# Optimization experiments

Hardware: AMD Instinct MI355X
Metric: run time of the kernel (lower is better)

The kernel has to match this reference:

```python
import jax, jax.numpy as jnp
import numpy as np

N_NODES = 100000
IN_FEATURES = 128
OUT_FEATURES = 128
N_EDGES = 3200000


def setup_inputs() -> dict:
    key = jax.random.key(0)
    k1, k2, k3, k4, k5 = jax.random.split(key, 5)
    node_features = jax.random.normal(k1, (N_NODES, IN_FEATURES), dtype=jnp.float32)
    edge_index = jax.random.randint(k2, (2, N_EDGES), 0, N_NODES, dtype=jnp.int64)
    edge_values = jax.random.uniform(k3, (N_EDGES,), dtype=jnp.float32)
    # Linear layer params (PyTorch nn.Linear: y = x @ W.T + b)
    bound = 1.0 / np.sqrt(IN_FEATURES)
    W = jax.random.uniform(k4, (OUT_FEATURES, IN_FEATURES), minval=-bound, maxval=bound, dtype=jnp.float32)
    b = jax.random.uniform(k5, (OUT_FEATURES,), minval=-bound, maxval=bound, dtype=jnp.float32)
    return {"node_features": node_features, "edge_index": edge_index,
            "edge_values": edge_values, "W": W, "b": b}


def reference(node_features, edge_index, edge_values, W, b):
    n_nodes = node_features.shape[0]
    row, col = edge_index[0], edge_index[1]
    # zero diagonal entries, then square edge values
    vals = jnp.where(row != col, edge_values, jnp.zeros_like(edge_values)) ** 2
    # linear transform: [N, F_out]
    wx = node_features @ W.T + b
    # SpMM: temp[i] = sum_e vals[e] * wx[col[e]] for row[e] == i
    messages = vals[:, None] * wx[col]          # [E, F_out] gather + scale
    temp = jax.ops.segment_sum(messages, row, num_segments=n_nodes)  # scatter-add
    # Hadamard product
    return wx * temp
```

## Files before the change

### kernel.cpp

```cpp
#include <hip/hip_runtime.h>
#include <hip/hip_bf16.h>

#define F 128
#define RB 196
#define NB_MAX 511
#define BIN_CAP 16
#define NBLK_BIN 512
#define NXS 16
#define NCG 16
#define KEYS (RB * NCG)

typedef __attribute__((ext_vector_type(8))) short bf16x8;
typedef __attribute__((ext_vector_type(4))) float f32x4;

static __device__ __forceinline__ unsigned short f2bfbits(float f) {
    __hip_bfloat16 h = __float2bfloat16(f);
    return __builtin_bit_cast(unsigned short, h);
}
static __device__ __forceinline__ short f2bf(float f) {
    __hip_bfloat16 h = __float2bfloat16(f);
    return __builtin_bit_cast(short, h);
}

__global__ __launch_bounds__(256) void gemm_mfma_kernel(
    const float* __restrict__ X, const float* __restrict__ W,
    const float* __restrict__ bias, float* __restrict__ wxf,
    __hip_bfloat16* __restrict__ wxh, int nrows, int writeF)
{
    __shared__ short xs[128][136];
    __shared__ short wt[128][136];
    __shared__ float bsh[128];

    int t = threadIdx.x;
    long row0 = (long)blockIdx.x * 128;

    {
        int r = t >> 1, h = t & 1;
        const float4* src = reinterpret_cast<const float4*>(W + r * F + h * 64);
#pragma unroll
        for (int i = 0; i < 16; ++i) {
            float4 v = src[i];
            short4 s;
            s.x = f2bf(v.x); s.y = f2bf(v.y); s.z = f2bf(v.z); s.w = f2bf(v.w);
            *reinterpret_cast<short4*>(&wt[r][h * 64 + i * 4]) = s;
        }
        if (t < 128) bsh[t] = bias[t];
    }
    {
        int r = t >> 1, h = t & 1;
        long gr = row0 + r; if (gr > nrows - 1) gr = nrows - 1;
        const float4* src = reinterpret_cast<const float4*>(X + gr * F + h * 64);
#pragma unroll
        for (int i = 0; i < 16; ++i) {
            float4 v = src[i];
            short4 s;
            s.x = f2bf(v.x); s.y = f2bf(v.y); s.z = f2bf(v.z); s.w = f2bf(v.w);
            *reinterpret_cast<short4*>(&xs[r][h * 64 + i * 4]) = s;
        }
    }
    __syncthreads();

    int wave = t >> 6, lane = t & 63;
    int l15 = lane & 15, lg = lane >> 4;
    int mrow = wave * 32;

    float bj[8];
#pragma unroll
    for (int nf = 0; nf < 8; ++nf) bj[nf] = bsh[nf * 16 + l15];

    f32x4 acc[2][8] = {};

#pragma unroll
    for (int ks = 0; ks < 4; ++ks) {
        bf16x8 a0 = *reinterpret_cast<const bf16x8*>(&xs[mrow + l15][ks * 32 + lg * 8]);
        bf16x8 a1 = *reinterpret_cast<const bf16x8*>(&xs[mrow + 16 + l15][ks * 32 + lg * 8]);
#pragma unroll
        for (int nf = 0; nf < 8; ++nf) {
            bf16x8 bfr = *reinterpret_cast<const bf16x8*>(&wt[nf * 16 + l15][ks * 32 + lg * 8]);
            acc[0][nf] = __builtin_amdgcn_mfma_f32_16x16x32_bf16(a0, bfr, acc[0][nf], 0, 0, 0);
            acc[1][nf] = __builtin_amdgcn_mfma_f32_16x16x32_bf16(a1, bfr, acc[1][nf], 0, 0, 0);
        }
    }

#pragma unroll
    for (int mf = 0; mf < 2; ++mf) {
#pragma unroll
        for (int i = 0; i < 4; ++i) {
            long grow = row0 + mrow + mf * 16 + lg * 4 + i;
            if (grow < nrows) {
#pragma unroll
                for (int nf = 0; nf < 8; ++nf) {
                    float v = acc[mf][nf][i] + bj[nf];
                    int col = nf * 16 + l15;
                    wxh[grow * F + col] = __float2bfloat16(v);
                    if (writeF) wxf[grow * F + col] = v;
                }
            }
        }
    }
}

__global__ __launch_bounds__(256) void bin_edges_kernel(
    const int* __restrict__ rowi, const int* __restrict__ coli,
    const float* __restrict__ ev, int* __restrict__ cur2,
    int2* __restrict__ arena1, int E, int NB, int CAPX)
{
    __shared__ int2 bins[NB_MAX][BIN_CAP];
    __shared__ int  cnt[NB_MAX];
    __shared__ int  flushed[NB_MAX];

    int t = threadIdx.x;
    int x = blockIdx.x & (NXS - 1);
    for (int i = t; i < NB; i += 256) { cnt[i] = 0; flushed[i] = 0; }
    __syncthreads();

    long per   = ((long)E + NBLK_BIN - 1) / NBLK_BIN;
    long start = (long)blockIdx.x * per;
    long endE  = start + per; if (endE > E) endE = E;

    int r = 0, c = 0; float v = 0.f;
    {
        long i0 = start + t;
        if (i0 < endE) { r = rowi[i0]; c = coli[i0]; v = ev[i0]; }
    }

    for (long base = start; base < endE; base += 256) {
        if (base + t < endE) {
            float v2 = (r != c) ? v * v : 0.0f;
            int b  = r / RB;
            int rl = r - b * RB;
            int pos = atomicAdd(&cnt[b], 1);
            bins[b][pos & (BIN_CAP - 1)] = make_int2((rl << 17) | c, __float_as_int(v2));
        }
        int rn = 0, cn = 0; float vn = 0.f;
        {
            long i2 = base + 256 + t;
            if (i2 < endE) { rn = rowi[i2]; cn = coli[i2]; vn = ev[i2]; }
        }
        __syncthreads();
        for (int bb = t; bb < NB; bb += 256) {
            while (cnt[bb] - flushed[bb] >= 8) {
                int gpos = atomicAdd(&cur2[x * NB + bb], 8);
                if (gpos + 8 <= CAPX) {
                    const int2* src = &bins[bb][flushed[bb] & (BIN_CAP - 1)];
                    int2* dst = &arena1[((size_t)x * NB + bb) * CAPX + gpos];
                    const int4* s4 = (const int4*)src;
                    int4* d4 = (int4*)dst;
                    d4[0] = s4[0]; d4[1] = s4[1]; d4[2] = s4[2]; d4[3] = s4[3];
                }
                flushed[bb] += 8;
            }
        }
        __syncthreads();
        r = rn; c = cn; v = vn;
    }
    for (int bb = t; bb < NB; bb += 256) {
        int rem = cnt[bb] - flushed[bb];
        if (rem > 0) {
            int gpos = atomicAdd(&cur2[x * NB + bb], rem);
            if (gpos + rem <= CAPX) {
                int2* dst = &arena1[((size_t)x * NB + bb) * CAPX + gpos];
                for (int k = 0; k < rem; ++k)
                    dst[k] = bins[bb][(flushed[bb] + k) & (BIN_CAP - 1)];
            }
        }
    }
}

__global__ __launch_bounds__(256) void sort_bucket_kernel(
    const int* __restrict__ cur2, const int2* __restrict__ arena1,
    unsigned int* __restrict__ arena2, int2* __restrict__ rowoff,
    int nrows, int NB, int CAPX, int CAP)
{
    __shared__ int koff[KEYS];
    __shared__ int sscan[256];

    int b = blockIdx.x;
    int t = threadIdx.x;
    unsigned int* dst = arena2 + (size_t)b * CAP;

    for (int i = t; i < KEYS; i += 256) koff[i] = 0;
    __syncthreads();

    for (int x = 0; x < NXS; ++x) {
        int n_x = cur2[x * NB + b]; if (n_x > CAPX) n_x = CAPX;
        const int2* seg = arena1 + ((size_t)x * NB + b) * CAPX;
        for (int i = t; i < n_x; i += 256) {
            int rx = seg[i].x;
            int key = (rx >> 17) * NCG + ((rx & 0x1FFFF) >> 13);
            atomicAdd(&koff[key], 1);
        }
    }
    __syncthreads();

    const int PER = (KEYS + 255) / 256;
    int lo = t * PER, hi = lo + PER; if (hi > KEYS) hi = KEYS; if (lo > KEYS) lo = KEYS;
    int s = 0;
    for (int i = lo; i < hi; ++i) s += koff[i];
    sscan[t] = s;
    __syncthreads();
#pragma unroll
    for (int d = 1; d < 256; d <<= 1) {
        int u = (t >= d) ? sscan[t - d] : 0;
        __syncthreads();
        sscan[t] += u;
        __syncthreads();
    }
    int total = sscan[255];
    int run = (t == 0) ? 0 : sscan[t - 1];
    for (int i = lo; i < hi; ++i) {
        int c0 = koff[i];
        koff[i] = run;
        run += c0;
    }
    __syncthreads();

    if (t < RB) {
        int grow = b * RB + t;
        if (grow < nrows) {
            int start = koff[t * NCG];
            int end   = (t == RB - 1) ? total : koff[(t + 1) * NCG];
            rowoff[grow] = make_int2(b * CAP + start, b * CAP + end);
        }
    }
    __syncthreads();

    for (int x = 0; x < NXS; ++x) {
        int n_x = cur2[x * NB + b]; if (n_x > CAPX) n_x = CAPX;
        const int2* seg = arena1 + ((size_t)x * NB + b) * CAPX;
        for (int i = t; i < n_x; i += 256) {
            int2 rec = seg[i];
            int c = rec.x & 0x1FFFF;
            int key = (rec.x >> 17) * NCG + (c >> 13);
            int pos = atomicAdd(&koff[key], 1);
            unsigned int pk = ((unsigned int)f2bfbits(__int_as_float(rec.y)) << 17)
                              | (unsigned int)c;
            if (pos < CAP) dst[pos] = pk;
        }
    }
}

__global__ __launch_bounds__(256) void agg_row_kernel(
    const int2* __restrict__ rowoff, const unsigned int* __restrict__ arena2,
    const unsigned int* __restrict__ wxh32, float* __restrict__ out,
    int nrows)
{
    int wid  = (blockIdx.x * 256 + threadIdx.x) >> 6;
    int lane = threadIdx.x & 63;
    if (wid >= nrows) return;

    int2 se   = rowoff[wid];
    int start = __builtin_amdgcn_readfirstlane(se.x);
    int end   = __builtin_amdgcn_readfirstlane(se.y);

    unsigned int gw = wxh32[(size_t)wid * 64 + lane];
    const unsigned int* wl = wxh32 + lane;

    float accx = 0.f, accy = 0.f;
    int e = start;
    for (; e + 7 < end; e += 8) {
        unsigned int p0 = arena2[e];
        unsigned int p1 = arena2[e + 1];
        unsigned int p2 = arena2[e + 2];
        unsigned int p3 = arena2[e + 3];
        unsigned int p4 = arena2[e + 4];
        unsigned int p5 = arena2[e + 5];
        unsigned int p6 = arena2[e + 6];
        unsigned int p7 = arena2[e + 7];
        unsigned int g0 = wl[(size_t)(p0 & 0x1FFFF) * 64];
        unsigned int g1 = wl[(size_t)(p1 & 0x1FFFF) * 64];
        unsigned int g2 = wl[(size_t)(p2 & 0x1FFFF) * 64];
        unsigned int g3 = wl[(size_t)(p3 & 0x1FFFF) * 64];
        unsigned int g4 = wl[(size_t)(p4 & 0x1FFFF) * 64];
        unsigned int g5 = wl[(size_t)(p5 & 0x1FFFF) * 64];
        unsigned int g6 = wl[(size_t)(p6 & 0x1FFFF) * 64];
        unsigned int g7 = wl[(size_t)(p7 & 0x1FFFF) * 64];
        float v0 = __uint_as_float((p0 >> 17) << 16);
        float v1 = __uint_as_float((p1 >> 17) << 16);
        float v2 = __uint_as_float((p2 >> 17) << 16);
        float v3 = __uint_as_float((p3 >> 17) << 16);
        float v4 = __uint_as_float((p4 >> 17) << 16);
        float v5 = __uint_as_float((p5 >> 17) << 16);
        float v6 = __uint_as_float((p6 >> 17) << 16);
        float v7 = __uint_as_float((p7 >> 17) << 16);
        accx = fmaf(v0, __uint_as_float(g0 << 16), accx);
        accy = fmaf(v0, __uint_as_float(g0 & 0xFFFF0000u), accy);
        accx = fmaf(v1, __uint_as_float(g1 << 16), accx);
        accy = fmaf(v1, __uint_as_float(g1 & 0xFFFF0000u), accy);
        accx = fmaf(v2, __uint_as_float(g2 << 16), accx);
        accy = fmaf(v2, __uint_as_float(g2 & 0xFFFF0000u), accy);
        accx = fmaf(v3, __uint_as_float(g3 << 16), accx);
        accy = fmaf(v3, __uint_as_float(g3 & 0xFFFF0000u), accy);
        accx = fmaf(v4, __uint_as_float(g4 << 16), accx);
        accy = fmaf(v4, __uint_as_float(g4 & 0xFFFF0000u), accy);
        accx = fmaf(v5, __uint_as_float(g5 << 16), accx);
        accy = fmaf(v5, __uint_as_float(g5 & 0xFFFF0000u), accy);
        accx = fmaf(v6, __uint_as_float(g6 << 16), accx);
        accy = fmaf(v6, __uint_as_float(g6 & 0xFFFF0000u), accy);
        accx = fmaf(v7, __uint_as_float(g7 << 16), accx);
        accy = fmaf(v7, __uint_as_float(g7 & 0xFFFF0000u), accy);
    }
    for (; e < end; ++e) {
        unsigned int p0 = arena2[e];
        unsigned int g0 = wl[(size_t)(p0 & 0x1FFFF) * 64];
        float v0 = __uint_as_float((p0 >> 17) << 16);
        accx = fmaf(v0, __uint_as_float(g0 << 16), accx);
        accy = fmaf(v0, __uint_as_float(g0 & 0xFFFF0000u), accy);
    }

    float2 o;
    o.x = __uint_as_float(gw << 16) * accx;
    o.y = __uint_as_float(gw & 0xFFFF0000u) * accy;
    *reinterpret_cast<float2*>(out + (size_t)wid * F + lane * 2) = o;
}

__global__ __launch_bounds__(256) void edge_scatter_kernel(
    const int* __restrict__ rowi, const int* __restrict__ coli,
    const float* __restrict__ ev, const float* __restrict__ wx,
    float* __restrict__ temp, int E)
{
    int tid = blockIdx.x * 256 + threadIdx.x;
    int e   = tid >> 5;
    if (e >= E) return;
    int lane = tid & 31;
    int r = rowi[e];
    int c = coli[e];
    if (r == c) return;
    float v = ev[e];
    v = v * v;
    const float4 wv = *reinterpret_cast<const float4*>(wx + (size_t)c * F + lane * 4);
    float* tp = temp + (size_t)r * F + lane * 4;
    atomicAdd(tp + 0, v * wv.x);
    atomicAdd(tp + 1, v * wv.y);
    atomicAdd(tp + 2, v * wv.z);
    atomicAdd(tp + 3, v * wv.w);
}

__global__ __launch_bounds__(256) void finalize_kernel(
    float* __restrict__ out, const float* __restrict__ temp, int n4)
{
    int i = blockIdx.x * 256 + threadIdx.x;
    if (i >= n4) return;
    float4 o  = reinterpret_cast<float4*>(out)[i];
    float4 tv = reinterpret_cast<const float4*>(temp)[i];
    o.x *= tv.x; o.y *= tv.y; o.z *= tv.z; o.w *= tv.w;
    reinterpret_cast<float4*>(out)[i] = o;
}

__global__ void Interaction_GraphConvolution_55963423867450_kernel() {}

extern "C" void kernel_launch(void* const* d_in, const int* in_sizes, int n_in,
                              void* d_out, int out_size, void* d_ws, size_t ws_size,
                              hipStream_t stream)
{
    const float* X  = (const float*)d_in[0];
    const int*   ei = (const int*)d_in[1];
    const float* ev = (const float*)d_in[2];
    const float* W  = (const float*)d_in[3];
    const float* b  = (const float*)d_in[4];
    float* out = (float*)d_out;

    int nrows = in_sizes[0] / F;
    int E     = in_sizes[2];
    const int* rowi = ei;
    const int* coli = ei + E;

    int gblocks = (int)((nrows + 127) / 128);

    int NB = (nrows + RB - 1) / RB;
    if (NB <= NB_MAX && nrows < (1 << 17)) {
        long avg = (long)E / NB;
        int CAP  = (int)(((avg * 9) / 8 + 192 + 7) & ~7L);
        int CAPX = (int)(((avg / NXS) * 5 / 4 + 64 + 7) & ~7L);

        char* p = (char*)d_ws;
        __hip_bfloat16* wxh = (__hip_bfloat16*)p;
        p += (size_t)nrows * F * sizeof(__hip_bfloat16);
        int* cur2 = (int*)p;
        p += (size_t)NXS * NB * sizeof(int);
        p = (char*)(((uintptr_t)p + 63) & ~(uintptr_t)63);
        int2* rowoff = (int2*)p;
        p += (size_t)nrows * sizeof(int2);
        int2* arena1 = (int2*)p;
        p += (size_t)NXS * NB * CAPX * sizeof(int2);
        unsigned int* arena2 = (unsigned int*)p;
        p += (size_t)NB * CAP * sizeof(unsigned int);
        size_t need = (size_t)(p - (char*)d_ws);

        if (ws_size >= need) {
            hipMemsetAsync(cur2, 0, (size_t)NXS * NB * sizeof(int), stream);
            gemm_mfma_kernel<<<gblocks, 256, 0, stream>>>(X, W, b, out, wxh, nrows, 0);
            bin_edges_kernel<<<NBLK_BIN, 256, 0, stream>>>(rowi, coli, ev, cur2,
                                                           arena1, E, NB, CAPX);
            sort_bucket_kernel<<<NB, 256, 0, stream>>>(cur2, arena1, arena2,
                                                       rowoff, nrows, NB, CAPX, CAP);
            int ablocks = (int)(((long)nrows * 64 + 255) / 256);
            agg_row_kernel<<<ablocks, 256, 0, stream>>>(rowoff, arena2,
                                                        (const unsigned int*)wxh,
                                                        out, nrows);
            return;
        }
    }

    float* temp = (float*)d_ws;
    hipMemsetAsync(temp, 0, (size_t)nrows * F * sizeof(float), stream);
    __hip_bfloat16* wxh_dummy = (__hip_bfloat16*)((char*)d_ws + (size_t)nrows * F * sizeof(float));
    gemm_mfma_kernel<<<(int)((nrows + 127) / 128), 256, 0, stream>>>(X, W, b, out, wxh_dummy, nrows, 1);
    long ethreads = (long)E * 32;
    int  eblocks32 = (int)((ethreads + 255) / 256);
    edge_scatter_kernel<<<eblocks32, 256, 0, stream>>>(rowi, coli, ev, out, temp, E);
    int n4 = nrows * F / 4;
    finalize_kernel<<<(n4 + 255) / 256, 256, 0, stream>>>(out, temp, n4);
}
```

Measured before the change: 214.2 us.

## Fuse GEMM and edge binning into one kernel, use nontemporal loads/stores

Merges the bf16 MFMA linear transform and the edge-binning pass into a single launch whose blocks take either role by interleaved groups of eight. GEMM blocks become persistent and loop over row tiles. The goal is to overlap the compute-bound GEMM with the memory-bound binning and save a launch. Separately, the streaming reads of the arenas and the final output stores become nontemporal to reduce cache pollution. The risk is that the larger shared-memory footprint lowers occupancy and the role split leaves load imbalance.

```diff
diff --git a/kernel.cpp b/kernel.cpp
--- a/kernel.cpp
+++ b/kernel.cpp
@@ -12,6 +12,8 @@
 
 typedef __attribute__((ext_vector_type(8))) short bf16x8;
 typedef __attribute__((ext_vector_type(4))) float f32x4;
+typedef __attribute__((ext_vector_type(2))) float f32x2;
+typedef __attribute__((ext_vector_type(2))) int   i32x2;
 
 static __device__ __forceinline__ unsigned short f2bfbits(float f) {
     __hip_bfloat16 h = __float2bfloat16(f);
@@ -22,18 +24,17 @@
     return __builtin_bit_cast(short, h);
 }
 
-__global__ __launch_bounds__(256) void gemm_mfma_kernel(
+__device__ __forceinline__ void gemm_role(
+    char* smem, int gid, int ntiles,
     const float* __restrict__ X, const float* __restrict__ W,
     const float* __restrict__ bias, float* __restrict__ wxf,
     __hip_bfloat16* __restrict__ wxh, int nrows, int writeF)
 {
-    __shared__ short xs[128][136];
-    __shared__ short wt[128][136];
-    __shared__ float bsh[128];
+    short (*xs)[136] = reinterpret_cast<short(*)[136]>(smem);
+    short (*wt)[136] = reinterpret_cast<short(*)[136]>(smem + 34816);
+    float* bsh       = reinterpret_cast<float*>(smem + 69632);
 
     int t = threadIdx.x;
-    long row0 = (long)blockIdx.x * 128;
-
     {
         int r = t >> 1, h = t & 1;
         const float4* src = reinterpret_cast<const float4*>(W + r * F + h * 64);
@@ -46,76 +47,81 @@
         }
         if (t < 128) bsh[t] = bias[t];
     }
-    {
-        int r = t >> 1, h = t & 1;
-        long gr = row0 + r; if (gr > nrows - 1) gr = nrows - 1;
-        const float4* src = reinterpret_cast<const float4*>(X + gr * F + h * 64);
-#pragma unroll
-        for (int i = 0; i < 16; ++i) {
-            float4 v = src[i];
-            short4 s;
-            s.x = f2bf(v.x); s.y = f2bf(v.y); s.z = f2bf(v.z); s.w = f2bf(v.w);
-            *reinterpret_cast<short4*>(&xs[r][h * 64 + i * 4]) = s;
-        }
-    }
-    __syncthreads();
 
     int wave = t >> 6, lane = t & 63;
     int l15 = lane & 15, lg = lane >> 4;
     int mrow = wave * 32;
 
-    float bj[8];
-#pragma unroll
-    for (int nf = 0; nf < 8; ++nf) bj[nf] = bsh[nf * 16 + l15];
-
-    f32x4 acc[2][8] = {};
-
-#pragma unroll
-    for (int ks = 0; ks < 4; ++ks) {
-        bf16x8 a0 = *reinterpret_cast<const bf16x8*>(&xs[mrow + l15][ks * 32 + lg * 8]);
-        bf16x8 a1 = *reinterpret_cast<const bf16x8*>(&xs[mrow + 16 + l15][ks * 32 + lg * 8]);
-#pragma unroll
-        for (int nf = 0; nf < 8; ++nf) {
-            bf16x8 bfr = *reinterpret_cast<const bf16x8*>(&wt[nf * 16 + l15][ks * 32 + lg * 8]);
-            acc[0][nf] = __builtin_amdgcn_mfma_f32_16x16x32_bf16(a0, bfr, acc[0][nf], 0, 0, 0);
-            acc[1][nf] = __builtin_amdgcn_mfma_f32_16x16x32_bf16(a1, bfr, acc[1][nf], 0, 0, 0);
-        }
-    }
-
-#pragma unroll
-    for (int mf = 0; mf < 2; ++mf) {
-#pragma unroll
-        for (int i = 0; i < 4; ++i) {
-            long grow = row0 + mrow + mf * 16 + lg * 4 + i;
-            if (grow < nrows) {
-#pragma unroll
-                for (int nf = 0; nf < 8; ++nf) {
-                    float v = acc[mf][nf][i] + bj[nf];
-                    int col = nf * 16 + l15;
-                    wxh[grow * F + col] = __float2bfloat16(v);
-                    if (writeF) wxf[grow * F + col] = v;
+    for (int tile = gid; tile < ntiles; tile += NBLK_BIN) {
+        long row0 = (long)tile * 128;
+        __syncthreads();
+        {
+            int r = t >> 1, h = t & 1;
+            long gr = row0 + r; if (gr > nrows - 1) gr = nrows - 1;
+            const float4* src = reinterpret_cast<const float4*>(X + gr * F + h * 64);
+#pragma unroll
+            for (int i = 0; i < 16; ++i) {
+                float4 v = src[i];
+                short4 s;
+                s.x = f2bf(v.x); s.y = f2bf(v.y); s.z = f2bf(v.z); s.w = f2bf(v.w);
+                *reinterpret_cast<short4*>(&xs[r][h * 64 + i * 4]) = s;
+            }
+        }
+        __syncthreads();
+
+        float bj[8];
+#pragma unroll
+        for (int nf = 0; nf < 8; ++nf) bj[nf] = bsh[nf * 16 + l15];
+
+        f32x4 acc[2][8] = {};
+#pragma unroll
+        for (int ks = 0; ks < 4; ++ks) {
+            bf16x8 a0 = *reinterpret_cast<const bf16x8*>(&xs[mrow + l15][ks * 32 + lg * 8]);
+            bf16x8 a1 = *reinterpret_cast<const bf16x8*>(&xs[mrow + 16 + l15][ks * 32 + lg * 8]);
+#pragma unroll
+            for (int nf = 0; nf < 8; ++nf) {
+                bf16x8 bfr = *reinterpret_cast<const bf16x8*>(&wt[nf * 16 + l15][ks * 32 + lg * 8]);
+                acc[0][nf] = __builtin_amdgcn_mfma_f32_16x16x32_bf16(a0, bfr, acc[0][nf], 0, 0, 0);
+                acc[1][nf] = __builtin_amdgcn_mfma_f32_16x16x32_bf16(a1, bfr, acc[1][nf], 0, 0, 0);
+            }
+        }
+
+#pragma unroll
+        for (int mf = 0; mf < 2; ++mf) {
+#pragma unroll
+            for (int i = 0; i < 4; ++i) {
+                long grow = row0 + mrow + mf * 16 + lg * 4 + i;
+                if (grow < nrows) {
+#pragma unroll
+                    for (int nf = 0; nf < 8; ++nf) {
+                        float v = acc[mf][nf][i] + bj[nf];
+                        int col = nf * 16 + l15;
+                        wxh[grow * F + col] = __float2bfloat16(v);
+                        if (writeF) wxf[grow * F + col] = v;
+                    }
                 }
             }
         }
     }
 }
 
-__global__ __launch_bounds__(256) void bin_edges_kernel(
+__device__ __forceinline__ void bin_role(
+    char* smem, int id,
     const int* __restrict__ rowi, const int* __restrict__ coli,
     const float* __restrict__ ev, int* __restrict__ cur2,
     int2* __restrict__ arena1, int E, int NB, int CAPX)
 {
-    __shared__ int2 bins[NB_MAX][BIN_CAP];
-    __shared__ int  cnt[NB_MAX];
-    __shared__ int  flushed[NB_MAX];
+    int2 (*bins)[BIN_CAP] = reinterpret_cast<int2(*)[BIN_CAP]>(smem);
+    int* cnt     = reinterpret_cast<int*>(smem + 65408);
+    int* flushed = reinterpret_cast<int*>(smem + 65408 + 2048);
 
     int t = threadIdx.x;
-    int x = blockIdx.x & (NXS - 1);
+    int x = id & (NXS - 1);
     for (int i = t; i < NB; i += 256) { cnt[i] = 0; flushed[i] = 0; }
     __syncthreads();
 
     long per   = ((long)E + NBLK_BIN - 1) / NBLK_BIN;
-    long start = (long)blockIdx.x * per;
+    long start = (long)id * per;
     long endE  = start + per; if (endE > E) endE = E;
 
     int r = 0, c = 0; float v = 0.f;
@@ -167,6 +173,33 @@
     }
 }
 
+__global__ __launch_bounds__(256) void fused_gemm_bin_kernel(
+    const float* __restrict__ X, const float* __restrict__ W,
+    const float* __restrict__ bias, __hip_bfloat16* __restrict__ wxh,
+    int nrows, int ntiles,
+    const int* __restrict__ rowi, const int* __restrict__ coli,
+    const float* __restrict__ ev, int* __restrict__ cur2,
+    int2* __restrict__ arena1, int E, int NB, int CAPX)
+{
+    __shared__ __align__(16) char smem[70656];
+    int b = blockIdx.x;
+    int group = b >> 3, within = b & 7;
+    int id = (group >> 1) * 8 + within;
+    if ((group & 1) == 0)
+        bin_role(smem, id, rowi, coli, ev, cur2, arena1, E, NB, CAPX);
+    else
+        gemm_role(smem, id, ntiles, X, W, bias, nullptr, wxh, nrows, 0);
+}
+
+__global__ __launch_bounds__(256) void gemm_mfma_kernel(
+    const float* __restrict__ X, const float* __restrict__ W,
+    const float* __restrict__ bias, float* __restrict__ wxf,
+    __hip_bfloat16* __restrict__ wxh, int nrows, int ntiles, int writeF)
+{
+    __shared__ __align__(16) char smem[70656];
+    gemm_role(smem, blockIdx.x, ntiles, X, W, bias, wxf, wxh, nrows, writeF);
+}
+
 __global__ __launch_bounds__(256) void sort_bucket_kernel(
     const int* __restrict__ cur2, const int2* __restrict__ arena1,
     unsigned int* __restrict__ arena2, int2* __restrict__ rowoff,
@@ -186,7 +219,8 @@
         int n_x = cur2[x * NB + b]; if (n_x > CAPX) n_x = CAPX;
         const int2* seg = arena1 + ((size_t)x * NB + b) * CAPX;
         for (int i = t; i < n_x; i += 256) {
-            int rx = seg[i].x;
+            i32x2 rv = __builtin_nontemporal_load(reinterpret_cast<const i32x2*>(seg + i));
+            int rx = rv[0];
             int key = (rx >> 17) * NCG + ((rx & 0x1FFFF) >> 13);
             atomicAdd(&koff[key], 1);
         }
@@ -229,11 +263,11 @@
         int n_x = cur2[x * NB + b]; if (n_x > CAPX) n_x = CAPX;
         const int2* seg = arena1 + ((size_t)x * NB + b) * CAPX;
         for (int i = t; i < n_x; i += 256) {
-            int2 rec = seg[i];
-            int c = rec.x & 0x1FFFF;
-            int key = (rec.x >> 17) * NCG + (c >> 13);
+            i32x2 rv = __builtin_nontemporal_load(reinterpret_cast<const i32x2*>(seg + i));
+            int c = rv[0] & 0x1FFFF;
+            int key = (rv[0] >> 17) * NCG + (c >> 13);
             int pos = atomicAdd(&koff[key], 1);
-            unsigned int pk = ((unsigned int)f2bfbits(__int_as_float(rec.y)) << 17)
+            unsigned int pk = ((unsigned int)f2bfbits(__int_as_float(rv[1])) << 17)
                               | (unsigned int)c;
             if (pos < CAP) dst[pos] = pk;
         }
@@ -259,14 +293,14 @@
     float accx = 0.f, accy = 0.f;
     int e = start;
     for (; e + 7 < end; e += 8) {
-        unsigned int p0 = arena2[e];
-        unsigned int p1 = arena2[e + 1];
-        unsigned int p2 = arena2[e + 2];
-        unsigned int p3 = arena2[e + 3];
-        unsigned int p4 = arena2[e + 4];
-        unsigned int p5 = arena2[e + 5];
-        unsigned int p6 = arena2[e + 6];
-        unsigned int p7 = arena2[e + 7];
+        unsigned int p0 = __builtin_nontemporal_load(arena2 + e);
+        unsigned int p1 = __builtin_nontemporal_load(arena2 + e + 1);
+        unsigned int p2 = __builtin_nontemporal_load(arena2 + e + 2);
+        unsigned int p3 = __builtin_nontemporal_load(arena2 + e + 3);
+        unsigned int p4 = __builtin_nontemporal_load(arena2 + e + 4);
+        unsigned int p5 = __builtin_nontemporal_load(arena2 + e + 5);
+        unsigned int p6 = __builtin_nontemporal_load(arena2 + e + 6);
+        unsigned int p7 = __builtin_nontemporal_load(arena2 + e + 7);
         unsigned int g0 = wl[(size_t)(p0 & 0x1FFFF) * 64];
         unsigned int g1 = wl[(size_t)(p1 & 0x1FFFF) * 64];
         unsigned int g2 = wl[(size_t)(p2 & 0x1FFFF) * 64];
@@ -301,17 +335,17 @@
         accy = fmaf(v7, __uint_as_float(g7 & 0xFFFF0000u), accy);
     }
     for (; e < end; ++e) {
-        unsigned int p0 = arena2[e];
+        unsigned int p0 = __builtin_nontemporal_load(arena2 + e);
         unsigned int g0 = wl[(size_t)(p0 & 0x1FFFF) * 64];
         float v0 = __uint_as_float((p0 >> 17) << 16);
         accx = fmaf(v0, __uint_as_float(g0 << 16), accx);
         accy = fmaf(v0, __uint_as_float(g0 & 0xFFFF0000u), accy);
     }
 
-    float2 o;
-    o.x = __uint_as_float(gw << 16) * accx;
-    o.y = __uint_as_float(gw & 0xFFFF0000u) * accy;
-    *reinterpret_cast<float2*>(out + (size_t)wid * F + lane * 2) = o;
+    f32x2 o;
+    o[0] = __uint_as_float(gw << 16) * accx;
+    o[1] = __uint_as_float(gw & 0xFFFF0000u) * accy;
+    __builtin_nontemporal_store(o, reinterpret_cast<f32x2*>(out + (size_t)wid * F + lane * 2));
 }
 
 __global__ __launch_bounds__(256) void edge_scatter_kernel(
@@ -365,7 +399,7 @@
     const int* rowi = ei;
     const int* coli = ei + E;
 
-    int gblocks = (int)((nrows + 127) / 128);
+    int ntiles = (nrows + 127) / 128;
 
     int NB = (nrows + RB - 1) / RB;
     if (NB <= NB_MAX && nrows < (1 << 17)) {
@@ -389,9 +423,9 @@
 
         if (ws_size >= need) {
             hipMemsetAsync(cur2, 0, (size_t)NXS * NB * sizeof(int), stream);
-            gemm_mfma_kernel<<<gblocks, 256, 0, stream>>>(X, W, b, out, wxh, nrows, 0);
-            bin_edges_kernel<<<NBLK_BIN, 256, 0, stream>>>(rowi, coli, ev, cur2,
-                                                           arena1, E, NB, CAPX);
+            fused_gemm_bin_kernel<<<2 * NBLK_BIN, 256, 0, stream>>>(
+                X, W, b, wxh, nrows, ntiles,
+                rowi, coli, ev, cur2, arena1, E, NB, CAPX);
             sort_bucket_kernel<<<NB, 256, 0, stream>>>(cur2, arena1, arena2,
                                                        rowoff, nrows, NB, CAPX, CAP);
             int ablocks = (int)(((long)nrows * 64 + 255) / 256);
@@ -405,7 +439,7 @@
     float* temp = (float*)d_ws;
     hipMemsetAsync(temp, 0, (size_t)nrows * F * sizeof(float), stream);
     __hip_bfloat16* wxh_dummy = (__hip_bfloat16*)((char*)d_ws + (size_t)nrows * F * sizeof(float));
-    gemm_mfma_kernel<<<(int)((nrows + 127) / 128), 256, 0, stream>>>(X, W, b, out, wxh_dummy, nrows, 1);
+    gemm_mfma_kernel<<<ntiles, 256, 0, stream>>>(X, W, b, out, wxh_dummy, nrows, ntiles, 1);
     long ethreads = (long)E * 32;
     int  eblocks32 = (int)((ethreads + 255) / 256);
     edge_scatter_kernel<<<eblocks32, 256, 0, stream>>>(rowi, coli, ev, out, temp, E);
```

Result: slower. 230.1 us (+7.4%).
